# Performance work log

Measured on AMD Instinct MI355X. Metric: run time of the kernel, lower is better.

Reference implementation:

```python
import jax, jax.numpy as jnp
import numpy as np

P, Q, B = 1024, 128, 64
HP, HQ, A = 1024, 1024, 75

def setup_inputs() -> dict:
    key = jax.random.key(0)
    ks = jax.random.split(key, 10)
    def w(k, shape, fan_in):
        return jax.random.uniform(k, shape, jnp.float32, -1.0, 1.0) / np.sqrt(fan_in)
    return {
        "h_passage": jax.random.normal(ks[0], (P, B, HP), jnp.float32),
        "u_question": jax.random.normal(ks[1], (Q, B, HQ), jnp.float32),
        "Whp": w(ks[2], (A, HP), HP),
        "Wha": w(ks[3], (A, HQ), HQ),
        "v_w": w(ks[4], (1, A), A),
        "Wuq": w(ks[5], (A, HQ), HQ),
        "v1_w": w(ks[6], (1, A), A),
        "v1_b": w(ks[7], (1,), A),
        "W_ih": w(ks[8], (3 * HQ, HP), HQ),  # GRUCell input->hidden, no bias
        "W_hh": w(ks[9], (3 * HQ, HQ), HQ),  # GRUCell hidden->hidden, no bias
    }

def gru_cell(x, h, W_ih, W_hh):
    # torch GRUCell (bias=False): gates ordered [r, z, n]
    gi = x @ W_ih.T            # (B, 3H)
    gh = h @ W_hh.T            # (B, 3H)
    i_r, i_z, i_n = jnp.split(gi, 3, axis=-1)
    h_r, h_z, h_n = jnp.split(gh, 3, axis=-1)
    r = jax.nn.sigmoid(i_r + h_r)
    z = jax.nn.sigmoid(i_z + h_z)
    n = jnp.tanh(i_n + r * h_n)
    return (1.0 - z) * n + z * h

def reference(h_passage, u_question, Whp, Wha, v_w, Wuq, v1_w, v1_b, W_ih, W_hh):
    # initial state: additive attention pooling over the question (axis 0)
    s = jnp.tanh(u_question @ Wuq.T) @ v1_w.T + v1_b      # (Q, B, 1)
    a = jax.nn.softmax(s, axis=0)
    ha0 = jnp.sum(a * u_question, axis=0)                 # (B, HQ)

    Wh = h_passage @ Whp.T                                # (P, B, A)

    s1 = jnp.tanh(Wh + ha0 @ Wha.T) @ v_w.T               # (P, B, 1)
    start_logits = jnp.transpose(s1, (1, 0, 2))           # (B, P, 1)
    a1 = jax.nn.softmax(s1, axis=0)
    c = jnp.sum(a1 * h_passage, axis=0)                   # (B, HP)
    ha1 = gru_cell(c, ha0, W_ih, W_hh)                    # (B, HQ)

    s2 = jnp.tanh(Wh + ha1 @ Wha.T) @ v_w.T               # (P, B, 1)
    end_logits = jnp.transpose(s2, (1, 0, 2))             # (B, P, 1)
    return (start_logits, end_logits)
```

## Files before the change

kernel.cpp:

```cpp
#include <hip/hip_runtime.h>
#include <math.h>

#define PP 1024
#define QQ 128
#define BB 64
#define HH 1024
#define AA 75
#define APAD 80
#define H3 3072
#define LDA 40

#define OFF_SQ    0L
#define OFF_AQ    8192L
#define OFF_HA0   16384L
#define OFF_HAW0  81920L
#define OFF_WH    87040L
#define OFF_S1    5329920L
#define OFF_A1    5395456L
#define OFF_C     5460992L
#define OFF_GI    5526528L
#define OFF_GH    5723136L
#define OFF_HA1   5919744L
#define OFF_HAW1  5985280L

typedef __attribute__((ext_vector_type(8))) __bf16 bf16x8;
typedef __attribute__((ext_vector_type(8))) unsigned short ushort8;
typedef __attribute__((ext_vector_type(4))) float f32x4;

__device__ __forceinline__ unsigned short f2bf(float x) {
    unsigned int u = __builtin_bit_cast(unsigned int, x);
    u += 0x7FFFu + ((u >> 16) & 1u);
    return (unsigned short)(u >> 16);
}
__device__ __forceinline__ float bf2f(unsigned short h) {
    unsigned int u = ((unsigned int)h) << 16;
    return __builtin_bit_cast(float, u);
}
__device__ __forceinline__ f32x4 mfma16(ushort8 a, ushort8 b, f32x4 c) {
    return __builtin_amdgcn_mfma_f32_16x16x32_bf16(
        __builtin_bit_cast(bf16x8, a), __builtin_bit_cast(bf16x8, b), c, 0, 0, 0);
}
__device__ __forceinline__ void split_store(unsigned short* hi, unsigned short* lo,
                                            int idx, float4 x) {
    ushort4 h, l;
    h.x = f2bf(x.x); l.x = f2bf(x.x - bf2f(h.x));
    h.y = f2bf(x.y); l.y = f2bf(x.y - bf2f(h.y));
    h.z = f2bf(x.z); l.z = f2bf(x.z - bf2f(h.z));
    h.w = f2bf(x.w); l.w = f2bf(x.w - bf2f(h.w));
    *reinterpret_cast<ushort4*>(hi + idx) = h;
    *reinterpret_cast<ushort4*>(lo + idx) = l;
}

template <bool ADD_HAW, bool STORE_RAW, bool ADD_BIAS>
__global__ __launch_bounds__(256) void gemm_attn(
    const float* __restrict__ X,
    const float* __restrict__ W,
    const float* __restrict__ haW,
    const float* __restrict__ vw,
    const float* __restrict__ bias,
    float* __restrict__ raw_out,
    float* __restrict__ s_out)
{
    __shared__ unsigned short Ah[128 * LDA], Al[128 * LDA];
    __shared__ unsigned short Bh[80 * LDA],  Bl[80 * LDA];

    const int t = threadIdx.x;
    const int row0 = blockIdx.x * 128;
    const int w = t >> 6;
    const int l = t & 63;
    const int lr = l & 15;
    const int lg = l >> 4;

    float vwv[5];
#pragma unroll
    for (int nt = 0; nt < 5; nt++) {
        const int col = lr + 16 * nt;
        vwv[nt] = (col < AA) ? vw[col] : 0.f;
    }

    f32x4 acc[2][5];
#pragma unroll
    for (int mt = 0; mt < 2; mt++)
#pragma unroll
        for (int nt = 0; nt < 5; nt++) acc[mt][nt] = (f32x4){0.f, 0.f, 0.f, 0.f};

    for (int k0 = 0; k0 < 1024; k0 += 32) {
        __syncthreads();
#pragma unroll
        for (int i = 0; i < 4; i++) {
            const int s = t + i * 256;
            const int row = s >> 3, kq = s & 7;
            const float4 x = *reinterpret_cast<const float4*>(
                X + (size_t)(row0 + row) * 1024 + k0 + kq * 4);
            split_store(Ah, Al, row * LDA + kq * 4, x);
        }
#pragma unroll
        for (int i = 0; i < 3; i++) {
            const int s = t + i * 256;
            if (s < 640) {
                const int a = s >> 3, kq = s & 7;
                float4 wv = make_float4(0.f, 0.f, 0.f, 0.f);
                if (a < AA)
                    wv = *reinterpret_cast<const float4*>(W + (size_t)a * 1024 + k0 + kq * 4);
                split_store(Bh, Bl, a * LDA + kq * 4, wv);
            }
        }
        __syncthreads();

        ushort8 ahm[2], alm[2];
#pragma unroll
        for (int mt = 0; mt < 2; mt++) {
            const int ar = (w * 32 + mt * 16 + lr) * LDA + lg * 8;
            ahm[mt] = *reinterpret_cast<const ushort8*>(&Ah[ar]);
            alm[mt] = *reinterpret_cast<const ushort8*>(&Al[ar]);
        }
#pragma unroll
        for (int nt = 0; nt < 5; nt++) {
            const int br = (nt * 16 + lr) * LDA + lg * 8;
            const ushort8 bh = *reinterpret_cast<const ushort8*>(&Bh[br]);
            const ushort8 bl = *reinterpret_cast<const ushort8*>(&Bl[br]);
#pragma unroll
            for (int mt = 0; mt < 2; mt++) {
                acc[mt][nt] = mfma16(ahm[mt], bh, acc[mt][nt]);
                acc[mt][nt] = mfma16(ahm[mt], bl, acc[mt][nt]);
                acc[mt][nt] = mfma16(alm[mt], bh, acc[mt][nt]);
            }
        }
    }

#pragma unroll
    for (int mt = 0; mt < 2; mt++) {
#pragma unroll
        for (int r = 0; r < 4; r++) {
            const int row_local = w * 32 + mt * 16 + lg * 4 + r;
            const int rg = row0 + row_local;
            const int b = rg & 63;
            float partial = 0.f;
#pragma unroll
            for (int nt = 0; nt < 5; nt++) {
                const int col = lr + 16 * nt;
                const float v = acc[mt][nt][r];
                if (STORE_RAW) raw_out[(size_t)rg * APAD + col] = v;
                if (col < AA) {
                    float hw = 0.f;
                    if (ADD_HAW) hw = haW[b * APAD + col];
                    partial += vwv[nt] * tanhf(v + hw);
                }
            }
            partial += __shfl_xor(partial, 1);
            partial += __shfl_xor(partial, 2);
            partial += __shfl_xor(partial, 4);
            partial += __shfl_xor(partial, 8);
            if (lr == 0) {
                if (ADD_BIAS) partial += bias[0];
                s_out[rg] = partial;
            }
        }
    }
}

__global__ __launch_bounds__(128) void softmax_q(const float* __restrict__ sq,
                                                 float* __restrict__ aq) {
    const int b = blockIdx.x;
    const int q = threadIdx.x;
    __shared__ float red[2], red2[2];
    float v = sq[q * BB + b];
    float m = v;
#pragma unroll
    for (int off = 1; off < 64; off <<= 1) m = fmaxf(m, __shfl_xor(m, off));
    if ((q & 63) == 0) red[q >> 6] = m;
    __syncthreads();
    m = fmaxf(red[0], red[1]);
    float e = expf(v - m);
    float s = e;
#pragma unroll
    for (int off = 1; off < 64; off <<= 1) s += __shfl_xor(s, off);
    if ((q & 63) == 0) red2[q >> 6] = s;
    __syncthreads();
    s = red2[0] + red2[1];
    aq[q * BB + b] = e / s;
}

__global__ __launch_bounds__(256) void pool_q(const float* __restrict__ u,
                                              const float* __restrict__ aq,
                                              float* __restrict__ ha0) {
    const int b = blockIdx.y;
    const int h = blockIdx.x * 256 + threadIdx.x;
    __shared__ float aw[QQ];
    if (threadIdx.x < QQ) aw[threadIdx.x] = aq[threadIdx.x * BB + b];
    __syncthreads();
    float acc = 0.f;
#pragma unroll 4
    for (int q = 0; q < QQ; q++)
        acc += aw[q] * u[(q * BB + b) * HH + h];
    ha0[b * HH + h] = acc;
}

__global__ __launch_bounds__(64) void vecmat(const float* __restrict__ x,
                                             const float* __restrict__ W,
                                             float* __restrict__ out) {
    const int a = blockIdx.x, b = blockIdx.y, l = threadIdx.x;
    float s = 0.f;
#pragma unroll 4
    for (int k = l; k < HH; k += 64) s += x[b * HH + k] * W[a * HH + k];
#pragma unroll
    for (int off = 1; off < 64; off <<= 1) s += __shfl_xor(s, off);
    if (l == 0) out[b * APAD + a] = s;
}

__global__ __launch_bounds__(256) void softmax_p(const float* __restrict__ s1,
                                                 float* __restrict__ a1,
                                                 float* __restrict__ outStart) {
    const int b = blockIdx.x;
    const int t = threadIdx.x;
    __shared__ float r4[4], r4b[4];
    float v[4];
    float m = -1e30f;
#pragma unroll
    for (int i = 0; i < 4; i++) {
        const int p = t + i * 256;
        v[i] = s1[p * BB + b];
        outStart[b * PP + p] = v[i];
        m = fmaxf(m, v[i]);
    }
#pragma unroll
    for (int off = 1; off < 64; off <<= 1) m = fmaxf(m, __shfl_xor(m, off));
    if ((t & 63) == 0) r4[t >> 6] = m;
    __syncthreads();
    m = fmaxf(fmaxf(r4[0], r4[1]), fmaxf(r4[2], r4[3]));
    float e[4];
    float s = 0.f;
#pragma unroll
    for (int i = 0; i < 4; i++) {
        e[i] = expf(v[i] - m);
        s += e[i];
    }
#pragma unroll
    for (int off = 1; off < 64; off <<= 1) s += __shfl_xor(s, off);
    if ((t & 63) == 0) r4b[t >> 6] = s;
    __syncthreads();
    s = r4b[0] + r4b[1] + r4b[2] + r4b[3];
    const float inv = 1.f / s;
#pragma unroll
    for (int i = 0; i < 4; i++) a1[(t + i * 256) * BB + b] = e[i] * inv;
}

__global__ __launch_bounds__(256) void weighted_pool_p(
    const float* __restrict__ hp, const float* __restrict__ a1,
    float* __restrict__ c) {
    const int b = blockIdx.y;
    const int h = blockIdx.x * 256 + threadIdx.x;
    const int ps = blockIdx.z;
    __shared__ float aw[128];
    if (threadIdx.x < 128) aw[threadIdx.x] = a1[(ps * 128 + threadIdx.x) * BB + b];
    __syncthreads();
    float acc = 0.f;
    const long base = ((long)ps * 128 * BB + b) * HH + h;
#pragma unroll 4
    for (int p = 0; p < 128; p++)
        acc += aw[p] * hp[base + (long)p * (BB * HH)];
    atomicAdd(&c[b * HH + h], acc);
}

__global__ __launch_bounds__(256) void gru_gemm(
    const float* __restrict__ c, const float* __restrict__ ha0,
    const float* __restrict__ W_ih, const float* __restrict__ W_hh,
    float* __restrict__ gi, float* __restrict__ gh) {
    const float* X = blockIdx.y ? ha0 : c;
    const float* W = blockIdx.y ? W_hh : W_ih;
    float* out = blockIdx.y ? gh : gi;
    const int n0 = blockIdx.x * 64;

    __shared__ unsigned short Ah[64 * LDA], Al[64 * LDA];
    __shared__ unsigned short Bh[64 * LDA], Bl[64 * LDA];

    const int t = threadIdx.x;
    const int w = t >> 6;
    const int l = t & 63;
    const int lr = l & 15;
    const int lg = l >> 4;

    f32x4 acc[4];
#pragma unroll
    for (int mt = 0; mt < 4; mt++) acc[mt] = (f32x4){0.f, 0.f, 0.f, 0.f};

    for (int k0 = 0; k0 < 1024; k0 += 32) {
        __syncthreads();
#pragma unroll
        for (int i = 0; i < 2; i++) {
            const int s = t + i * 256;
            const int row = s >> 3, kq = s & 7;
            const float4 x = *reinterpret_cast<const float4*>(
                X + (size_t)row * 1024 + k0 + kq * 4);
            split_store(Ah, Al, row * LDA + kq * 4, x);
            const float4 wv = *reinterpret_cast<const float4*>(
                W + (size_t)(n0 + row) * 1024 + k0 + kq * 4);
            split_store(Bh, Bl, row * LDA + kq * 4, wv);
        }
        __syncthreads();

        const int br = (w * 16 + lr) * LDA + lg * 8;
        const ushort8 bh = *reinterpret_cast<const ushort8*>(&Bh[br]);
        const ushort8 bl = *reinterpret_cast<const ushort8*>(&Bl[br]);
#pragma unroll
        for (int mt = 0; mt < 4; mt++) {
            const int ar = (mt * 16 + lr) * LDA + lg * 8;
            const ushort8 ah = *reinterpret_cast<const ushort8*>(&Ah[ar]);
            const ushort8 al = *reinterpret_cast<const ushort8*>(&Al[ar]);
            acc[mt] = mfma16(ah, bh, acc[mt]);
            acc[mt] = mfma16(ah, bl, acc[mt]);
            acc[mt] = mfma16(al, bh, acc[mt]);
        }
    }

#pragma unroll
    for (int mt = 0; mt < 4; mt++)
#pragma unroll
        for (int r = 0; r < 4; r++) {
            const int row = mt * 16 + lg * 4 + r;
            const int n = n0 + w * 16 + lr;
            out[(size_t)row * H3 + n] = acc[mt][r];
        }
}

__global__ __launch_bounds__(256) void gru_gate(const float* __restrict__ gi,
                                                const float* __restrict__ gh,
                                                const float* __restrict__ ha0,
                                                float* __restrict__ ha1) {
    const int b = blockIdx.y;
    const int hn = blockIdx.x * 256 + threadIdx.x;
    const long o = (long)b * H3 + hn;
    const float r = 1.f / (1.f + expf(-(gi[o] + gh[o])));
    const float z = 1.f / (1.f + expf(-(gi[o + 1024] + gh[o + 1024])));
    const float n = tanhf(gi[o + 2048] + r * gh[o + 2048]);
    ha1[b * HH + hn] = (1.f - z) * n + z * ha0[b * HH + hn];
}

__global__ __launch_bounds__(256) void end_logits_k(
    const float* __restrict__ wh, const float* __restrict__ haW1,
    const float* __restrict__ vw, float* __restrict__ out) {
    const int row0 = blockIdx.x * 64;
    const int t = threadIdx.x;
    const int l = t & 15;
    const int rbase = (t >> 4) * 4;
#pragma unroll
    for (int i = 0; i < 4; i++) {
        const int r = row0 + rbase + i;
        const int b = r & 63;
        float partial = 0.f;
#pragma unroll
        for (int j = 0; j < 5; j++) {
            const int col = l + 16 * j;
            if (col < AA)
                partial +=
                    vw[col] * tanhf(wh[(size_t)r * APAD + col] + haW1[b * APAD + col]);
        }
        partial += __shfl_xor(partial, 1);
        partial += __shfl_xor(partial, 2);
        partial += __shfl_xor(partial, 4);
        partial += __shfl_xor(partial, 8);
        if (l == 0) {
            const int p = r >> 6;
            out[(size_t)BB * PP + b * PP + p] = partial;
        }
    }
}

extern "C" void kernel_launch(void* const* d_in, const int* in_sizes, int n_in,
                              void* d_out, int out_size, void* d_ws,
                              size_t ws_size, hipStream_t stream) {
    const float* hp   = (const float*)d_in[0];
    const float* u    = (const float*)d_in[1];
    const float* Whp  = (const float*)d_in[2];
    const float* Wha  = (const float*)d_in[3];
    const float* v_w  = (const float*)d_in[4];
    const float* Wuq  = (const float*)d_in[5];
    const float* v1w  = (const float*)d_in[6];
    const float* v1b  = (const float*)d_in[7];
    const float* W_ih = (const float*)d_in[8];
    const float* W_hh = (const float*)d_in[9];
    float* out = (float*)d_out;
    float* ws = (float*)d_ws;

    hipLaunchKernelGGL((gemm_attn<false, false, true>), dim3(QQ * BB / 128),
                       dim3(256), 0, stream, u, Wuq, nullptr, v1w, v1b, nullptr,
                       ws + OFF_SQ);
    hipLaunchKernelGGL(softmax_q, dim3(BB), dim3(128), 0, stream, ws + OFF_SQ,
                       ws + OFF_AQ);
    hipLaunchKernelGGL(pool_q, dim3(HH / 256, BB), dim3(256), 0, stream, u,
                       ws + OFF_AQ, ws + OFF_HA0);
    hipLaunchKernelGGL(vecmat, dim3(AA, BB), dim3(64), 0, stream, ws + OFF_HA0,
                       Wha, ws + OFF_HAW0);
    hipLaunchKernelGGL((gemm_attn<true, true, false>), dim3(PP * BB / 128),
                       dim3(256), 0, stream, hp, Whp, ws + OFF_HAW0, v_w,
                       nullptr, ws + OFF_WH, ws + OFF_S1);
    hipLaunchKernelGGL(softmax_p, dim3(BB), dim3(256), 0, stream, ws + OFF_S1,
                       ws + OFF_A1, out);
    hipMemsetAsync(ws + OFF_C, 0, (size_t)BB * HH * sizeof(float), stream);
    hipLaunchKernelGGL(weighted_pool_p, dim3(HH / 256, BB, 8), dim3(256), 0,
                       stream, hp, ws + OFF_A1, ws + OFF_C);
    hipLaunchKernelGGL(gru_gemm, dim3(H3 / 64, 2), dim3(256), 0, stream,
                       ws + OFF_C, ws + OFF_HA0, W_ih, W_hh, ws + OFF_GI,
                       ws + OFF_GH);
    hipLaunchKernelGGL(gru_gate, dim3(HH / 256, BB), dim3(256), 0, stream,
                       ws + OFF_GI, ws + OFF_GH, ws + OFF_HA0, ws + OFF_HA1);
    hipLaunchKernelGGL(vecmat, dim3(AA, BB), dim3(64), 0, stream, ws + OFF_HA1,
                       Wha, ws + OFF_HAW1);
    hipLaunchKernelGGL(end_logits_k, dim3(PP * BB / 64), dim3(256), 0, stream,
                       ws + OFF_WH, ws + OFF_HAW1, v_w, out);
    (void)in_sizes; (void)n_in; (void)out_size; (void)ws_size;
}
```

Before: 718.6 us.

## Pre-split weights to bf16 hi/lo and pipeline GEMM loads via global_load_lds

Adds a split_w kernel that converts Whp and Wuq once per call into a tiled bf16 hi/lo layout in workspace, so the attention GEMM no longer splits weights per block. The GEMM now loads X and weight tiles straight into LDS with global_load_lds using a swizzled layout, double-buffered for X and triple-buffered for weights, with explicit vmcnt waits so the next tile's loads overlap compute. It also switches the float-to-bf16 conversion to native casts. The cost is two extra small launches, workspace reuse of the GI/GH regions, and a single s_barrier per tile, which raises the risk of LDS races.

```diff
diff --git a/kernel.cpp b/kernel.cpp
--- a/kernel.cpp
+++ b/kernel.cpp
@@ -8,6 +8,9 @@
 #define AA 75
 #define APAD 80
 #define H3 3072
+#define BM 128
+#define BK 32
+#define NTILE 32
 #define LDA 40
 
 #define OFF_SQ    0L
@@ -40,36 +43,74 @@
     return __builtin_amdgcn_mfma_f32_16x16x32_bf16(
         __builtin_bit_cast(bf16x8, a), __builtin_bit_cast(bf16x8, b), c, 0, 0, 0);
 }
+__device__ __forceinline__ void cvt_hilo4(const float4 x, ushort4& h, ushort4& lo) {
+    __bf16 a = (__bf16)x.x, b = (__bf16)x.y, c = (__bf16)x.z, d = (__bf16)x.w;
+    h.x = __builtin_bit_cast(unsigned short, a);
+    h.y = __builtin_bit_cast(unsigned short, b);
+    h.z = __builtin_bit_cast(unsigned short, c);
+    h.w = __builtin_bit_cast(unsigned short, d);
+    lo.x = __builtin_bit_cast(unsigned short, (__bf16)(x.x - (float)a));
+    lo.y = __builtin_bit_cast(unsigned short, (__bf16)(x.y - (float)b));
+    lo.z = __builtin_bit_cast(unsigned short, (__bf16)(x.z - (float)c));
+    lo.w = __builtin_bit_cast(unsigned short, (__bf16)(x.w - (float)d));
+}
+__device__ __forceinline__ void gl2lds16(const void* g, void* s) {
+    __builtin_amdgcn_global_load_lds(
+        (const __attribute__((address_space(1))) unsigned int*)g,
+        (__attribute__((address_space(3))) unsigned int*)s, 16, 0, 0);
+}
 __device__ __forceinline__ void split_store(unsigned short* hi, unsigned short* lo,
                                             int idx, float4 x) {
     ushort4 h, l;
-    h.x = f2bf(x.x); l.x = f2bf(x.x - bf2f(h.x));
-    h.y = f2bf(x.y); l.y = f2bf(x.y - bf2f(h.y));
-    h.z = f2bf(x.z); l.z = f2bf(x.z - bf2f(h.z));
-    h.w = f2bf(x.w); l.w = f2bf(x.w - bf2f(h.w));
+    cvt_hilo4(x, h, l);
     *reinterpret_cast<ushort4*>(hi + idx) = h;
     *reinterpret_cast<ushort4*>(lo + idx) = l;
+}
+
+__global__ __launch_bounds__(256) void split_w(const float* __restrict__ Wsrc,
+                                               unsigned short* __restrict__ dst) {
+    const int n = blockIdx.x * 256 + threadIdx.x;
+    const int a = n % 80;
+    const int kg = (n / 80) & 3;
+    const int hl = (n / 320) & 1;
+    const int tile = n / 640;
+    const int k = tile * 32 + kg * 8;
+    float4 x0 = make_float4(0.f, 0.f, 0.f, 0.f), x1 = x0;
+    if (a < AA) {
+        x0 = *reinterpret_cast<const float4*>(Wsrc + (size_t)a * 1024 + k);
+        x1 = *reinterpret_cast<const float4*>(Wsrc + (size_t)a * 1024 + k + 4);
+    }
+    ushort4 h0, l0, h1, l1;
+    cvt_hilo4(x0, h0, l0);
+    cvt_hilo4(x1, h1, l1);
+    ushort8 o;
+    if (hl == 0) { o[0]=h0.x; o[1]=h0.y; o[2]=h0.z; o[3]=h0.w; o[4]=h1.x; o[5]=h1.y; o[6]=h1.z; o[7]=h1.w; }
+    else         { o[0]=l0.x; o[1]=l0.y; o[2]=l0.z; o[3]=l0.w; o[4]=l1.x; o[5]=l1.y; o[6]=l1.z; o[7]=l1.w; }
+    *reinterpret_cast<ushort8*>(dst + (size_t)n * 8) = o;
 }
 
 template <bool ADD_HAW, bool STORE_RAW, bool ADD_BIAS>
 __global__ __launch_bounds__(256) void gemm_attn(
     const float* __restrict__ X,
-    const float* __restrict__ W,
+    const unsigned short* __restrict__ Wsp,
     const float* __restrict__ haW,
     const float* __restrict__ vw,
     const float* __restrict__ bias,
     float* __restrict__ raw_out,
     float* __restrict__ s_out)
 {
-    __shared__ unsigned short Ah[128 * LDA], Al[128 * LDA];
-    __shared__ unsigned short Bh[80 * LDA],  Bl[80 * LDA];
+    __shared__ __align__(16) float X32[2][BM][BK];
+    __shared__ __align__(16) unsigned short Xbf[2][4][BM][8];
+    __shared__ __align__(16) unsigned short Bsh[3][5120];
 
     const int t = threadIdx.x;
-    const int row0 = blockIdx.x * 128;
     const int w = t >> 6;
     const int l = t & 63;
     const int lr = l & 15;
     const int lg = l >> 4;
+    const int l3 = l >> 3;
+    const int l7 = l & 7;
+    const int row0 = blockIdx.x * BM;
 
     float vwv[5];
 #pragma unroll
@@ -77,6 +118,7 @@
         const int col = lr + 16 * nt;
         vwv[nt] = (col < AA) ? vw[col] : 0.f;
     }
+    asm volatile("s_waitcnt vmcnt(0)" ::: "memory");
 
     f32x4 acc[2][5];
 #pragma unroll
@@ -84,49 +126,76 @@
 #pragma unroll
         for (int nt = 0; nt < 5; nt++) acc[mt][nt] = (f32x4){0.f, 0.f, 0.f, 0.f};
 
-    for (int k0 = 0; k0 < 1024; k0 += 32) {
-        __syncthreads();
+    const int swz = (l7 ^ l3);
+
+#define ISSUE_X(tile, buf)                                                      \
+    {                                                                           \
+        _Pragma("unroll")                                                       \
+        for (int c = 0; c < 4; c++) {                                           \
+            const int r = w * 32 + c * 8 + l3;                                  \
+            const float* src = X + (size_t)(row0 + r) * 1024 + (tile) * BK + swz * 4; \
+            gl2lds16(src, &X32[buf][w * 32 + c * 8][0]);                        \
+        }                                                                       \
+    }
+#define ISSUE_B(tile, bufb)                                                     \
+    {                                                                           \
+        _Pragma("unroll")                                                       \
+        for (int j = 0; j < 3; j++) {                                           \
+            int cc = w * 3 + j;                                                 \
+            if (cc >= 10) cc -= 10;                 \
+            const unsigned short* src = Wsp + (size_t)(tile) * 5120 + cc * 512 + l * 8; \
+            gl2lds16(src, &Bsh[bufb][cc * 512]);                                \
+        }                                                                       \
+    }
+
+    ISSUE_X(0, 0);
+    ISSUE_B(0, 0);
+
+    for (int tt = 0; tt < NTILE; ++tt) {
+        const int cur = tt & 1;
+        const int bufB = tt % 3;
+        if (tt + 1 < NTILE) {
+            ISSUE_X(tt + 1, cur ^ 1);
+            ISSUE_B(tt + 1, (tt + 1) % 3);
+            asm volatile("s_waitcnt vmcnt(7)" ::: "memory");
+        } else {
+            asm volatile("s_waitcnt vmcnt(0)" ::: "memory");
+        }
+        __builtin_amdgcn_sched_barrier(0);
+
 #pragma unroll
         for (int i = 0; i < 4; i++) {
-            const int s = t + i * 256;
-            const int row = s >> 3, kq = s & 7;
-            const float4 x = *reinterpret_cast<const float4*>(
-                X + (size_t)(row0 + row) * 1024 + k0 + kq * 4);
-            split_store(Ah, Al, row * LDA + kq * 4, x);
-        }
-#pragma unroll
-        for (int i = 0; i < 3; i++) {
-            const int s = t + i * 256;
-            if (s < 640) {
-                const int a = s >> 3, kq = s & 7;
-                float4 wv = make_float4(0.f, 0.f, 0.f, 0.f);
-                if (a < AA)
-                    wv = *reinterpret_cast<const float4*>(W + (size_t)a * 1024 + k0 + kq * 4);
-                split_store(Bh, Bl, a * LDA + kq * 4, wv);
-            }
-        }
-        __syncthreads();
-
-        ushort8 ahm[2], alm[2];
-#pragma unroll
-        for (int mt = 0; mt < 2; mt++) {
-            const int ar = (w * 32 + mt * 16 + lr) * LDA + lg * 8;
-            ahm[mt] = *reinterpret_cast<const ushort8*>(&Ah[ar]);
-            alm[mt] = *reinterpret_cast<const ushort8*>(&Al[ar]);
-        }
+            const int r = w * 32 + i * 8 + l3;
+            const float4 x = *reinterpret_cast<const float4*>(&X32[cur][r][swz * 4]);
+            ushort4 h, lo;
+            cvt_hilo4(x, h, lo);
+            const int kg = l7 >> 1, hf = (l7 & 1) * 4;
+            *reinterpret_cast<ushort4*>(&Xbf[0][kg][r][hf]) = h;
+            *reinterpret_cast<ushort4*>(&Xbf[1][kg][r][hf]) = lo;
+        }
+
+        asm volatile("s_barrier" ::: "memory");
+
+        ushort8 ah0h, ah0l, ah1h, ah1l;
+        ah0h = *reinterpret_cast<const ushort8*>(&Xbf[0][lg][w * 32 + 0 + lr][0]);
+        ah0l = *reinterpret_cast<const ushort8*>(&Xbf[1][lg][w * 32 + 0 + lr][0]);
+        ah1h = *reinterpret_cast<const ushort8*>(&Xbf[0][lg][w * 32 + 16 + lr][0]);
+        ah1l = *reinterpret_cast<const ushort8*>(&Xbf[1][lg][w * 32 + 16 + lr][0]);
 #pragma unroll
         for (int nt = 0; nt < 5; nt++) {
-            const int br = (nt * 16 + lr) * LDA + lg * 8;
-            const ushort8 bh = *reinterpret_cast<const ushort8*>(&Bh[br]);
-            const ushort8 bl = *reinterpret_cast<const ushort8*>(&Bl[br]);
-#pragma unroll
-            for (int mt = 0; mt < 2; mt++) {
-                acc[mt][nt] = mfma16(ahm[mt], bh, acc[mt][nt]);
-                acc[mt][nt] = mfma16(ahm[mt], bl, acc[mt][nt]);
-                acc[mt][nt] = mfma16(alm[mt], bh, acc[mt][nt]);
-            }
-        }
-    }
+            const int aoff = lg * 640 + (nt * 16 + lr) * 8;
+            const ushort8 bh = *reinterpret_cast<const ushort8*>(&Bsh[bufB][aoff]);
+            const ushort8 bl = *reinterpret_cast<const ushort8*>(&Bsh[bufB][2560 + aoff]);
+            acc[0][nt] = mfma16(ah0h, bh, acc[0][nt]);
+            acc[0][nt] = mfma16(ah0h, bl, acc[0][nt]);
+            acc[0][nt] = mfma16(ah0l, bh, acc[0][nt]);
+            acc[1][nt] = mfma16(ah1h, bh, acc[1][nt]);
+            acc[1][nt] = mfma16(ah1h, bl, acc[1][nt]);
+            acc[1][nt] = mfma16(ah1l, bh, acc[1][nt]);
+        }
+    }
+#undef ISSUE_X
+#undef ISSUE_B
 
 #pragma unroll
     for (int mt = 0; mt < 2; mt++) {
@@ -381,18 +450,22 @@
     const float* W_hh = (const float*)d_in[9];
     float* out = (float*)d_out;
     float* ws = (float*)d_ws;
-
-    hipLaunchKernelGGL((gemm_attn<false, false, true>), dim3(QQ * BB / 128),
-                       dim3(256), 0, stream, u, Wuq, nullptr, v1w, v1b, nullptr,
-                       ws + OFF_SQ);
+    unsigned short* wsp_hp = (unsigned short*)(ws + OFF_GI);
+    unsigned short* wsp_uq = (unsigned short*)(ws + OFF_GH);
+
+    hipLaunchKernelGGL(split_w, dim3(80), dim3(256), 0, stream, Whp, wsp_hp);
+    hipLaunchKernelGGL(split_w, dim3(80), dim3(256), 0, stream, Wuq, wsp_uq);
+    hipLaunchKernelGGL((gemm_attn<false, false, true>), dim3(QQ * BB / BM),
+                       dim3(256), 0, stream, u, wsp_uq, nullptr, v1w, v1b,
+                       nullptr, ws + OFF_SQ);
     hipLaunchKernelGGL(softmax_q, dim3(BB), dim3(128), 0, stream, ws + OFF_SQ,
                        ws + OFF_AQ);
     hipLaunchKernelGGL(pool_q, dim3(HH / 256, BB), dim3(256), 0, stream, u,
                        ws + OFF_AQ, ws + OFF_HA0);
     hipLaunchKernelGGL(vecmat, dim3(AA, BB), dim3(64), 0, stream, ws + OFF_HA0,
                        Wha, ws + OFF_HAW0);
-    hipLaunchKernelGGL((gemm_attn<true, true, false>), dim3(PP * BB / 128),
-                       dim3(256), 0, stream, hp, Whp, ws + OFF_HAW0, v_w,
+    hipLaunchKernelGGL((gemm_attn<true, true, false>), dim3(PP * BB / BM),
+                       dim3(256), 0, stream, hp, wsp_hp, ws + OFF_HAW0, v_w,
                        nullptr, ws + OFF_WH, ws + OFF_S1);
     hipLaunchKernelGGL(softmax_p, dim3(BB), dim3(256), 0, stream, ws + OFF_S1,
                        ws + OFF_A1, out);
```

Measured after the change: 624.2 us. -13.1%, faster.
